# Kernel optimization log

Measured on AMD Instinct MI355X. Metric: run time of the kernel, lower is better.

## Reference

```python
import jax, jax.numpy as jnp
import numpy as np

NUM_HEADS = 16


def setup_inputs() -> dict:
    key = jax.random.key(0)
    k1, k2, k3, k4, k5 = jax.random.split(key, 5)
    B, N, C = 4, 1370, 1024
    s = 0.02
    return {
        "tokens": jax.random.normal(k1, (B, N, C), jnp.float32),
        "qkv_w": jax.random.normal(k2, (3 * C, C), jnp.float32) * s,
        "qkv_b": jax.random.normal(k3, (3 * C,), jnp.float32) * s,
        "proj_w": jax.random.normal(k4, (C, C), jnp.float32) * s,
        "proj_b": jax.random.normal(k5, (C,), jnp.float32) * s,
    }


def reference(tokens, qkv_w, qkv_b, proj_w, proj_b):
    B, N, C = tokens.shape
    H = NUM_HEADS
    c = C // H
    scale = c ** (-0.5)
    # qkv projection: [B,N,3C] -> [3,B,H,N,c]
    qkv = tokens @ qkv_w.T + qkv_b
    qkv = qkv.reshape(B, N, 3, H, c).transpose(2, 0, 3, 1, 4)
    q, k, v = qkv[0], qkv[1], qkv[2]
    q = q * scale
    attn = jnp.einsum("bhqc,bhkc->bhqk", q, k)  # [B,H,N,N]
    w = jax.nn.softmax(attn, axis=-1)
    out = jnp.einsum("bhqk,bhkc->bhqc", w, v)  # [B,H,N,c]
    out = out.transpose(0, 2, 1, 3).reshape(B, N, C)
    return out @ proj_w.T + proj_b
```

## Files before the change

### kernel.cpp

```cpp
#include <hip/hip_runtime.h>
#include <hip/hip_bf16.h>

typedef short s16x8 __attribute__((ext_vector_type(8)));
typedef float f32x4 __attribute__((ext_vector_type(4)));
typedef float f32x16 __attribute__((ext_vector_type(16)));
typedef unsigned short u16;
typedef unsigned int   u32;
typedef u16 u16x4 __attribute__((ext_vector_type(4)));

#define SEQ  1370
#define CH   1024
#define NH   16
#define HD   64
#define BN   5480
#define MPAD 5504
#define NPAD 1408
#define NQT  43
#define NKT64 22

#define QSCALE 0.18033688f


__device__ __forceinline__ u16 f2bf(float f){
  union { float f; unsigned u; } v; v.f = f;
  unsigned u = v.u;
  return (u16)((u + 0x7FFFu + ((u >> 16) & 1u)) >> 16);
}

__device__ __forceinline__ u32 cvt_pk_bf16(float lo, float hi){
  u32 r;
  asm("v_cvt_pk_bf16_f32 %0, %1, %2" : "=v"(r) : "v"(lo), "v"(hi));
  return r;
}

#define GLOAD16(gp, lp) __builtin_amdgcn_global_load_lds( \
    (const __attribute__((address_space(1))) void*)(gp), \
    (__attribute__((address_space(3))) void*)(lp), 16, 0, 0)

__global__ __launch_bounds__(256) void k_cast_tokens(const float* __restrict__ in, u16* __restrict__ out){
  int i = blockIdx.x * 256 + threadIdx.x;
  if(i >= MPAD*CH) return;
  int row = i >> 10;
  out[i] = (row < BN) ? f2bf(in[i]) : (u16)0;
}

__global__ __launch_bounds__(256) void k_cast(const float* __restrict__ in, u16* __restrict__ out, int n){
  int i = blockIdx.x * 256 + threadIdx.x;
  if(i < n) out[i] = f2bf(in[i]);
}

template<int MODE, int NT>
__global__ __launch_bounds__(256,2) void k_gemm128(
    const u16* __restrict__ A, const u16* __restrict__ Bw, const float* __restrict__ bias,
    u16* __restrict__ q, u16* __restrict__ kk_, u16* __restrict__ vv, float* __restrict__ out)
{
  constexpr int NF = NT/32;
  constexpr int BJ = NT/32;
  __shared__ u16 As[128*64];
  __shared__ u16 Bs[NT*64];
  const int t = threadIdx.x;
  const int lane = t & 63;
  const int w = t >> 6;
  const int wm = w >> 1, wn = w & 1;
  const int g = lane >> 4, lr = lane & 15;

  const int bid = blockIdx.x;
  const int xcd = bid & 7, idx = bid >> 3;
  const int xr = xcd & 3, yr = xcd >> 2;
  constexpr int YLOC = (MODE == 0) ? 12 : 8;
  const int x = xr*11 + idx % 11;
  const int y = yr*YLOC + idx / 11;
  if(x >= MPAD/128) return;
  const int m0 = x*128, n0 = y*NT;

  const int swc = ((t & 7) ^ ((t >> 3) & 7)) * 8;
  const u16* ga0 = A  + (size_t)(m0 + (t >> 3)) * 1024 + swc;
  const u16* gb0 = Bw + (size_t)(n0 + (t >> 3)) * 1024 + swc;

  f32x4 z = {0.f,0.f,0.f,0.f};
  f32x4 acc[4][NF];
#pragma unroll
  for(int mf=0;mf<4;mf++)
#pragma unroll
    for(int nf=0;nf<NF;nf++) acc[mf][nf] = z;

  for(int k0 = 0; k0 < 1024; k0 += 64){
#pragma unroll
    for(int j=0;j<4;j++)
      GLOAD16(ga0 + k0 + j*32*1024, As + j*2048 + w*512);
#pragma unroll
    for(int j=0;j<BJ;j++)
      GLOAD16(gb0 + k0 + j*32*1024, Bs + j*2048 + w*512);
    __syncthreads();
#pragma unroll
    for(int kk=0; kk<2; kk++){
      s16x8 af[4], bf[NF];
#pragma unroll
      for(int mf = 0; mf < 4; mf++)
        af[mf] = *reinterpret_cast<const s16x8*>(&As[(wm*64 + mf*16 + lr)*64 + ((kk*4+g) ^ (lr&7))*8]);
#pragma unroll
      for(int nf = 0; nf < NF; nf++)
        bf[nf] = *reinterpret_cast<const s16x8*>(&Bs[(wn*16*NF + nf*16 + lr)*64 + ((kk*4+g) ^ (lr&7))*8]);
#pragma unroll
      for(int mf = 0; mf < 4; mf++)
#pragma unroll
        for(int nf = 0; nf < NF; nf++)
          acc[mf][nf] = __builtin_amdgcn_mfma_f32_16x16x32_bf16(af[mf], bf[nf], acc[mf][nf], 0,0,0);
    }
    __syncthreads();
  }

#pragma unroll
  for(int mf = 0; mf < 4; mf++){
#pragma unroll
    for(int nf = 0; nf < NF; nf++){
      int colc = n0 + wn*16*NF + nf*16 + lr;
      float bb = bias[colc];
#pragma unroll
      for(int r = 0; r < 4; r++){
        int row = m0 + wm*64 + mf*16 + g*4 + r;
        if(row >= BN) continue;
        float v = acc[mf][nf][r] + bb;
        if constexpr (MODE == 0){
          int b = row / SEQ, n = row - b*SEQ;
          int tt = colc >> 10, h = (colc >> 6) & 15, cc = colc & 63;
          int bh = b*NH + h;
          if(tt == 2){
            int ktv = n >> 6, kh = (n >> 4) & 3, hiv = (n >> 3) & 1, e = n & 7;
            int dtv = cc >> 5, colr = cc & 31;
            vv[(size_t)((((bh*22 + ktv)*4 + kh)*2 + dtv)*2 + hiv)*256 + colr*8 + e] = f2bf(v);
          } else {
            int gg = n >> 5, colr = n & 31;
            int dtv = cc >> 4, hiq = (cc >> 3) & 1, e = cc & 7;
            size_t fidx = (size_t)(((bh*44 + gg)*4 + dtv)*2 + hiq)*256 + colr*8 + e;
            if(tt == 0) q  [fidx] = f2bf(v * QSCALE);
            else        kk_[fidx] = f2bf(v);
          }
        } else {
          out[(size_t)row * CH + colc] = v;
        }
      }
    }
  }
}

__global__ __launch_bounds__(256,3) void k_attn6(
    const u16* __restrict__ Qf, const u16* __restrict__ Kf,
    const u16* __restrict__ Vf, u16* __restrict__ O)
{
  const int bid = blockIdx.x;
  const int swz = (bid & 7)*88 + (bid >> 3);
  const int bh = swz / 11;
  const int qg = swz - bh*11;
  const int w = threadIdx.x >> 6;
  int qt = qg*4 + w;
  const bool wr = (qt < NQT);
  if(!wr) qt = NQT - 1;
  const int lane = threadIdx.x & 63;
  const int col = lane & 31;
  const int hi  = lane >> 5;
  const int n0  = qt * 32;
  const size_t lofs = hi*256 + col*8;

  s16x8 qf[4];
  {
    const u16* qfb = Qf + (size_t)(bh*44 + qt)*2048 + lofs;
#pragma unroll
    for(int dt=0; dt<4; dt++)
      qf[dt] = *reinterpret_cast<const s16x8*>(qfb + dt*512);
  }
  const u16* kfb = Kf + (size_t)bh*44*2048 + lofs;
  const u16* vfb = Vf + (size_t)bh*22*4096 + lofs;

  f32x16 accO[2];
#pragma unroll
  for(int i=0;i<16;i++){ accO[0][i]=0.f; accO[1][i]=0.f; }
  float m_run = -1e30f, l_run = 0.f;

  for(int kt = 0; kt < NKT64; kt++){
    const int kj0 = kt * 64;
    __builtin_amdgcn_s_barrier();
    f32x16 St[2];
    __builtin_amdgcn_s_setprio(1);
#pragma unroll
    for(int s=0;s<2;s++){
#pragma unroll
      for(int i=0;i<16;i++) St[s][i]=0.f;
      const u16* kr = kfb + (size_t)(kt*2+s)*2048;
#pragma unroll
      for(int dt=0;dt<4;dt++){
        s16x8 kf = *reinterpret_cast<const s16x8*>(kr + dt*512);
        St[s] = __builtin_amdgcn_mfma_f32_32x32x16_bf16(kf, qf[dt], St[s], 0,0,0);
      }
    }
    __builtin_amdgcn_s_setprio(0);
    s16x8 vfr[8];
    {
      const u16* vr = vfb + (size_t)kt*4096;
#pragma unroll
      for(int i=0;i<8;i++)
        vfr[i] = *reinterpret_cast<const s16x8*>(vr + i*512);
    }
    float p[32];
    if(kj0 + 64 <= SEQ){
#pragma unroll
      for(int i=0;i<32;i++) p[i] = St[i>>4][i&15];
    } else {
#pragma unroll
      for(int s=0;s<2;s++)
#pragma unroll
        for(int r=0;r<16;r++){
          int k = kj0 + s*32 + (r&3) + 8*(r>>2) + 4*hi;
          p[s*16+r] = (k < SEQ) ? St[s][r] : -1e30f;
        }
    }
    float red[16];
#pragma unroll
    for(int i=0;i<16;i++) red[i] = fmaxf(p[i], p[i+16]);
#pragma unroll
    for(int s2=8;s2>=1;s2>>=1)
#pragma unroll
      for(int i=0;i<8;i++) if(i<s2) red[i] = fmaxf(red[i], red[i+s2]);
    float mx = fmaxf(red[0], __shfl_xor(red[0], 32));
    if(!__all(mx <= m_run + 8.f)){
      float mnew = fmaxf(m_run, mx);
      float alpha = exp2f(m_run - mnew);
      m_run = mnew;
      l_run *= alpha;
#pragma unroll
      for(int i=0;i<16;i++){ accO[0][i]*=alpha; accO[1][i]*=alpha; }
    }
#pragma unroll
    for(int i=0;i<32;i++) p[i] = exp2f(p[i] - m_run);
    float sr[16];
#pragma unroll
    for(int i=0;i<16;i++) sr[i] = p[i] + p[i+16];
#pragma unroll
    for(int s2=8;s2>=1;s2>>=1)
#pragma unroll
      for(int i=0;i<8;i++) if(i<s2) sr[i] += sr[i+s2];
    l_run += sr[0] + __shfl_xor(sr[0], 32);
    union PF { u32 w[4]; s16x8 v; } pf[4];
#pragma unroll
    for(int s=0;s<2;s++){
#pragma unroll
      for(int hh=0; hh<2; hh++){
        const int b0 = s*16 + hh*8;
        u32 w0 = cvt_pk_bf16(p[b0+0], p[b0+1]);
        u32 w1 = cvt_pk_bf16(p[b0+2], p[b0+3]);
        u32 w2 = cvt_pk_bf16(p[b0+4], p[b0+5]);
        u32 w3 = cvt_pk_bf16(p[b0+6], p[b0+7]);
        auto r02 = __builtin_amdgcn_permlane32_swap(w0, w2, false, false);
        auto r13 = __builtin_amdgcn_permlane32_swap(w1, w3, false, false);
        pf[s*2+hh].w[0] = r02[0];
        pf[s*2+hh].w[1] = r13[0];
        pf[s*2+hh].w[2] = r02[1];
        pf[s*2+hh].w[3] = r13[1];
      }
    }
    __builtin_amdgcn_s_setprio(1);
#pragma unroll
    for(int kh=0; kh<4; kh++)
#pragma unroll
      for(int dt=0; dt<2; dt++)
        accO[dt] = __builtin_amdgcn_mfma_f32_32x32x16_bf16(vfr[kh*2+dt], pf[kh].v, accO[dt], 0,0,0);
    __builtin_amdgcn_s_setprio(0);
  }

  const int n = n0 + col;
  if(wr && n < SEQ){
    float inv = 1.0f / l_run;
    const int b = bh >> 4, h = bh & 15;
    u16* orow = O + ((size_t)(b*SEQ + n))*CH + h*HD;
#pragma unroll
    for(int dt=0; dt<2; dt++)
#pragma unroll
      for(int qd=0; qd<4; qd++){
        u16x4 ov;
#pragma unroll
        for(int j=0;j<4;j++) ov[j] = f2bf(accO[dt][qd*4+j]*inv);
        *reinterpret_cast<u16x4*>(orow + dt*32 + qd*8 + hi*4) = ov;
      }
  }
}

extern "C" void kernel_launch(void* const* d_in, const int* in_sizes, int n_in,
                              void* d_out, int out_size, void* d_ws, size_t ws_size,
                              hipStream_t stream)
{
  const float* tokens = (const float*)d_in[0];
  const float* qkv_w  = (const float*)d_in[1];
  const float* qkv_b  = (const float*)d_in[2];
  const float* proj_w = (const float*)d_in[3];
  const float* proj_b = (const float*)d_in[4];
  float* out = (float*)d_out;

  char* ws = (char*)d_ws;
  u16* Xbf   = (u16*)(ws);
  u16* Wqkv  = (u16*)(ws + 11272192);
  u16* Wproj = (u16*)(ws + 17563648);
  u16* Qfb   = (u16*)(ws + 19660800);
  u16* Kfb   = (u16*)(ws + 31195136);
  u16* Vfb   = (u16*)(ws + 42729472);
  u16* AttO  = (u16*)(ws + 65798144);

  k_cast_tokens<<<dim3((MPAD*CH)/256), 256, 0, stream>>>(tokens, Xbf);
  k_cast<<<dim3((3*CH*CH)/256), 256, 0, stream>>>(qkv_w, Wqkv, 3*CH*CH);
  k_cast<<<dim3((CH*CH)/256),   256, 0, stream>>>(proj_w, Wproj, CH*CH);

  k_gemm128<0,128><<<dim3(1056), 256, 0, stream>>>(Xbf, Wqkv, qkv_b, Qfb, Kfb, Vfb, nullptr);
  k_attn6<<<dim3(704), 256, 0, stream>>>(Qfb, Kfb, Vfb, AttO);
  k_gemm128<1,64><<<dim3(704), 256, 0, stream>>>(AttO, Wproj, proj_b, nullptr, nullptr, nullptr, out);
}
```

Measured before the change: 182.2 us.

## Double-buffer LDS tiles in GEMM and stage K/V through shared memory in attention

Measured after the change: 184.9 us. Within noise of the previous version (+1.5%).

```diff
diff --git a/kernel.cpp b/kernel.cpp
--- a/kernel.cpp
+++ b/kernel.cpp
@@ -55,9 +55,8 @@
     u16* __restrict__ q, u16* __restrict__ kk_, u16* __restrict__ vv, float* __restrict__ out)
 {
   constexpr int NF = NT/32;
-  constexpr int BJ = NT/32;
-  __shared__ u16 As[128*64];
-  __shared__ u16 Bs[NT*64];
+  __shared__ u16 As[2][128*64];
+  __shared__ u16 Bs[2][NT*64];
   const int t = threadIdx.x;
   const int lane = t & 63;
   const int w = t >> 6;
@@ -77,6 +76,12 @@
   const u16* ga0 = A  + (size_t)(m0 + (t >> 3)) * 1024 + swc;
   const u16* gb0 = Bw + (size_t)(n0 + (t >> 3)) * 1024 + swc;
 
+#define STAGE_G(K0, CB) { \
+  _Pragma("unroll") \
+  for(int j=0;j<4;j++) GLOAD16(ga0 + (K0) + j*32*1024, &As[CB][j*2048 + w*512]); \
+  _Pragma("unroll") \
+  for(int j=0;j<NF;j++) GLOAD16(gb0 + (K0) + j*32*1024, &Bs[CB][j*2048 + w*512]); }
+
   f32x4 z = {0.f,0.f,0.f,0.f};
   f32x4 acc[4][NF];
 #pragma unroll
@@ -84,23 +89,20 @@
 #pragma unroll
     for(int nf=0;nf<NF;nf++) acc[mf][nf] = z;
 
+  STAGE_G(0, 0);
+  __syncthreads();
   for(int k0 = 0; k0 < 1024; k0 += 64){
-#pragma unroll
-    for(int j=0;j<4;j++)
-      GLOAD16(ga0 + k0 + j*32*1024, As + j*2048 + w*512);
-#pragma unroll
-    for(int j=0;j<BJ;j++)
-      GLOAD16(gb0 + k0 + j*32*1024, Bs + j*2048 + w*512);
-    __syncthreads();
+    const int cur = (k0 >> 6) & 1;
+    if(k0 + 64 < 1024) STAGE_G(k0 + 64, cur^1);
 #pragma unroll
     for(int kk=0; kk<2; kk++){
       s16x8 af[4], bf[NF];
 #pragma unroll
       for(int mf = 0; mf < 4; mf++)
-        af[mf] = *reinterpret_cast<const s16x8*>(&As[(wm*64 + mf*16 + lr)*64 + ((kk*4+g) ^ (lr&7))*8]);
+        af[mf] = *reinterpret_cast<const s16x8*>(&As[cur][(wm*64 + mf*16 + lr)*64 + ((kk*4+g) ^ (lr&7))*8]);
 #pragma unroll
       for(int nf = 0; nf < NF; nf++)
-        bf[nf] = *reinterpret_cast<const s16x8*>(&Bs[(wn*16*NF + nf*16 + lr)*64 + ((kk*4+g) ^ (lr&7))*8]);
+        bf[nf] = *reinterpret_cast<const s16x8*>(&Bs[cur][(wn*16*NF + nf*16 + lr)*64 + ((kk*4+g) ^ (lr&7))*8]);
 #pragma unroll
       for(int mf = 0; mf < 4; mf++)
 #pragma unroll
@@ -144,10 +146,12 @@
   }
 }
 
-__global__ __launch_bounds__(256,3) void k_attn6(
+__global__ __launch_bounds__(256,3) void k_attn7(
     const u16* __restrict__ Qf, const u16* __restrict__ Kf,
     const u16* __restrict__ Vf, u16* __restrict__ O)
 {
+  __shared__ u16 Kl[2][4096];
+  __shared__ u16 Vl[2][4096];
   const int bid = blockIdx.x;
   const int swz = (bid & 7)*88 + (bid >> 3);
   const int bh = swz / 11;
@@ -160,7 +164,7 @@
   const int col = lane & 31;
   const int hi  = lane >> 5;
   const int n0  = qt * 32;
-  const size_t lofs = hi*256 + col*8;
+  const int lofs = hi*256 + col*8;
 
   s16x8 qf[4];
   {
@@ -169,38 +173,43 @@
     for(int dt=0; dt<4; dt++)
       qf[dt] = *reinterpret_cast<const s16x8*>(qfb + dt*512);
   }
-  const u16* kfb = Kf + (size_t)bh*44*2048 + lofs;
-  const u16* vfb = Vf + (size_t)bh*22*4096 + lofs;
+  const u16* kfb = Kf + (size_t)bh*44*2048;
+  const u16* vfb = Vf + (size_t)bh*22*4096;
+
+#define STAGE_T(KT, CB) { \
+  const u16* gk_ = kfb + (size_t)(KT)*4096 + w*1024 + lane*8; \
+  const u16* gv_ = vfb + (size_t)(KT)*4096 + w*1024 + lane*8; \
+  GLOAD16(gk_,       &Kl[CB][w*1024]); \
+  GLOAD16(gk_ + 512, &Kl[CB][w*1024 + 512]); \
+  GLOAD16(gv_,       &Vl[CB][w*1024]); \
+  GLOAD16(gv_ + 512, &Vl[CB][w*1024 + 512]); }
 
   f32x16 accO[2];
 #pragma unroll
   for(int i=0;i<16;i++){ accO[0][i]=0.f; accO[1][i]=0.f; }
   float m_run = -1e30f, l_run = 0.f;
 
+  STAGE_T(0, 0);
+  asm volatile("s_waitcnt vmcnt(0)" ::: "memory");
+  __builtin_amdgcn_s_barrier();
+
   for(int kt = 0; kt < NKT64; kt++){
     const int kj0 = kt * 64;
-    __builtin_amdgcn_s_barrier();
+    const int cur = kt & 1;
+    if(kt + 1 < NKT64) STAGE_T(kt + 1, cur^1);
     f32x16 St[2];
     __builtin_amdgcn_s_setprio(1);
 #pragma unroll
     for(int s=0;s<2;s++){
 #pragma unroll
       for(int i=0;i<16;i++) St[s][i]=0.f;
-      const u16* kr = kfb + (size_t)(kt*2+s)*2048;
 #pragma unroll
       for(int dt=0;dt<4;dt++){
-        s16x8 kf = *reinterpret_cast<const s16x8*>(kr + dt*512);
+        s16x8 kf = *reinterpret_cast<const s16x8*>(&Kl[cur][s*2048 + dt*512 + lofs]);
         St[s] = __builtin_amdgcn_mfma_f32_32x32x16_bf16(kf, qf[dt], St[s], 0,0,0);
       }
     }
     __builtin_amdgcn_s_setprio(0);
-    s16x8 vfr[8];
-    {
-      const u16* vr = vfb + (size_t)kt*4096;
-#pragma unroll
-      for(int i=0;i<8;i++)
-        vfr[i] = *reinterpret_cast<const s16x8*>(vr + i*512);
-    }
     float p[32];
     if(kj0 + 64 <= SEQ){
 #pragma unroll
@@ -262,9 +271,13 @@
 #pragma unroll
     for(int kh=0; kh<4; kh++)
 #pragma unroll
-      for(int dt=0; dt<2; dt++)
-        accO[dt] = __builtin_amdgcn_mfma_f32_32x32x16_bf16(vfr[kh*2+dt], pf[kh].v, accO[dt], 0,0,0);
+      for(int dt=0; dt<2; dt++){
+        s16x8 vf = *reinterpret_cast<const s16x8*>(&Vl[cur][(kh*2+dt)*512 + lofs]);
+        accO[dt] = __builtin_amdgcn_mfma_f32_32x32x16_bf16(vf, pf[kh].v, accO[dt], 0,0,0);
+      }
     __builtin_amdgcn_s_setprio(0);
+    asm volatile("s_waitcnt vmcnt(0)" ::: "memory");
+    __builtin_amdgcn_s_barrier();
   }
 
   const int n = n0 + col;
@@ -309,6 +322,6 @@
   k_cast<<<dim3((CH*CH)/256),   256, 0, stream>>>(proj_w, Wproj, CH*CH);
 
   k_gemm128<0,128><<<dim3(1056), 256, 0, stream>>>(Xbf, Wqkv, qkv_b, Qfb, Kfb, Vfb, nullptr);
-  k_attn6<<<dim3(704), 256, 0, stream>>>(Qfb, Kfb, Vfb, AttO);
+  k_attn7<<<dim3(704), 256, 0, stream>>>(Qfb, Kfb, Vfb, AttO);
   k_gemm128<1,64><<<dim3(704), 256, 0, stream>>>(AttO, Wproj, proj_b, nullptr, nullptr, nullptr, out);
 }
```
